# Performance work log

Measured on AMD Instinct MI355X. Metric: run time of the kernel, lower is better.

Reference implementation:

```python
import jax, jax.numpy as jnp
import numpy as np

N = 200000          # active input voxels
GRID = 96           # voxel grid extent
_OFFS = np.array([[dx, dy, dz] for dx in (-1, 0, 1) for dy in (-1, 0, 1) for dz in (-1, 0, 1)], dtype=np.int64)  # 27 kernel offsets


def _build_kmap(cin, cout, stride):
    """Build gather/scatter kernel maps for a 3x3x3 sparse conv.
    For each offset k and each output j, find input i with coord_in[i] == coord_out[j]*stride + off[k].
    Misses scatter to sentinel row n_out (dropped) and gather row 0 (value ignored)."""
    B = int(max(cin.max(), cout.max() * stride + 1)) + 3
    key_in = (cin[:, 0].astype(np.int64) * B + cin[:, 1]) * B + cin[:, 2]
    order = np.argsort(key_in).astype(np.int32)
    sk = key_in[order]
    n_out = cout.shape[0]
    g = np.zeros((27, n_out), np.int32)
    s = np.full((27, n_out), n_out, np.int32)
    ar = np.arange(n_out, dtype=np.int32)
    co = cout.astype(np.int64)
    for k in range(27):
        q = co * stride + _OFFS[k]
        valid = (q >= 0).all(axis=1)
        qk = (q[:, 0] * B + q[:, 1]) * B + q[:, 2]
        pos = np.clip(np.searchsorted(sk, qk), 0, sk.shape[0] - 1)
        found = valid & (sk[pos] == qk)
        g[k] = np.where(found, order[pos], 0)
        s[k] = np.where(found, ar, n_out)
    return jnp.asarray(g), jnp.asarray(s)


def setup_inputs() -> dict:
    rng = np.random.RandomState(0)
    raw = rng.randint(0, GRID, size=(3 * N, 3))
    coords = np.unique(raw, axis=0)[:N]          # [N,3] unique voxel coords
    c1 = coords
    c2 = np.unique(c1 // 2, axis=0)              # stride-2 output coords
    g1, s1 = _build_kmap(c1, c1, 1)              # submanifold conv1
    g2, s2 = _build_kmap(c1, c2, 2)              # strided conv2
    g3, s3 = _build_kmap(c2, c2, 1)              # submanifold conv3
    key = jax.random.key(0)
    k1, k2, k3, k4 = jax.random.split(key, 4)
    feats = jax.random.normal(k1, (N, 4), jnp.float32)
    W1 = jax.random.normal(k2, (27, 4, 32), jnp.float32) * (1.0 / np.sqrt(27 * 4))
    W2 = jax.random.normal(k3, (27, 32, 32), jnp.float32) * (1.0 / np.sqrt(27 * 32))
    W3 = jax.random.normal(k4, (27, 32, 2), jnp.float32) * (1.0 / np.sqrt(27 * 32))
    return {"feats": feats, "W1": W1, "W2": W2, "W3": W3,
            "g1": g1, "s1": s1, "g2": g2, "s2": s2, "g3": g3, "s3": s3}


def _sparse_conv(feats, W, gidx, sidx):
    n_out = sidx.shape[1]
    c_out = W.shape[-1]
    gathered = feats[gidx]                              # [27, M, Cin] irregular gather
    contrib = jnp.einsum('kmc,kcd->kmd', gathered, W)   # per-offset GEMM
    out = jnp.zeros((n_out + 1, c_out), feats.dtype)    # +1 sentinel row for misses
    out = out.at[sidx.reshape(-1)].add(contrib.reshape(-1, c_out))  # scatter-add
    return out[:n_out]


def reference(feats, W1, W2, W3, g1, s1, g2, s2, g3, s3):
    x = _sparse_conv(feats, W1, g1, s1)
    x = _sparse_conv(x, W2, g2, s2)
    x = _sparse_conv(x, W3, g3, s3)
    return x
```

## Files before the change

kernel.cpp:

```cpp
#include <hip/hip_runtime.h>

#define CDIV(a,b) (((a)+(b)-1)/(b))

typedef __attribute__((ext_vector_type(8))) short short8v;
typedef __attribute__((ext_vector_type(4))) short short4v;
typedef __attribute__((ext_vector_type(4))) float f32x4;

__device__ inline unsigned short f2bf(float x) {
    unsigned u = __builtin_bit_cast(unsigned, x);
    u += 0x7fffu + ((u >> 16) & 1u);
    return (unsigned short)(u >> 16);
}

__global__ __launch_bounds__(256) void prep_feats_k(
    const float* __restrict__ feats, unsigned short* __restrict__ featsh,
    unsigned short* __restrict__ x1h, int N)
{
    int i = blockIdx.x * 256 + threadIdx.x;
    if (i < N) {
        float4 f = *reinterpret_cast<const float4*>(feats + (size_t)i * 4);
        ushort4 h; h.x = f2bf(f.x); h.y = f2bf(f.y); h.z = f2bf(f.z); h.w = f2bf(f.w);
        *reinterpret_cast<ushort4*>(featsh + (size_t)i * 4) = h;
    } else if (i == N) {
        *reinterpret_cast<ushort4*>(featsh + (size_t)N * 4) = make_ushort4(0, 0, 0, 0);
        #pragma unroll
        for (int t = 0; t < 8; ++t)
            *reinterpret_cast<ushort4*>(x1h + (size_t)N * 32 + t * 4) = make_ushort4(0, 0, 0, 0);
    }
}

__global__ __launch_bounds__(256) void prep_w_k(
    const float* __restrict__ W1, const float* __restrict__ W2,
    unsigned short* __restrict__ w2h, unsigned short* __restrict__ w1f)
{
    int i = blockIdx.x * 256 + threadIdx.x;
    if (i < 27 * 1024) {
        int k = i >> 10, c = (i >> 5) & 31, d = i & 31;
        w2h[k * 1024 + d * 32 + c] = f2bf(W2[i]);
    } else if (i < 27 * 1024 + 4096) {
        int idx = i - 27 * 1024;
        int mf = idx >> 10, n = (idx >> 5) & 31, kc = idx & 31;
        int slot = mf * 8 + (kc >> 2), c = kc & 3;
        float v = (slot < 27) ? W1[slot * 128 + c * 32 + n] : 0.f;
        w1f[mf * 1024 + n * 32 + kc] = f2bf(v);
    }
}

__global__ __launch_bounds__(256, 6) void conv1_k(
    const unsigned short* __restrict__ featsh, const unsigned short* __restrict__ w1f,
    const int* __restrict__ g1, const int* __restrict__ s1,
    unsigned short* __restrict__ x1h, int N)
{
    int tid = threadIdx.x;
    int l = tid & 63, wv = tid >> 6;
    int lr = l & 15, kq = l >> 4;
    int rbase = blockIdx.x * 64 + wv * 16;
    int j = rbase + lr;
    int jc = j < N ? j : N - 1;

    int gm[4][2];
    #pragma unroll
    for (int mf = 0; mf < 4; ++mf)
        #pragma unroll
        for (int t = 0; t < 2; ++t) {
            int slot = mf * 8 + kq * 2 + t;
            int v = N;
            if (slot < 27 && j < N) {
                int s = s1[(size_t)slot * N + jc];
                int g = g1[(size_t)slot * N + jc];
                v = (s != N) ? g : N;
            }
            gm[mf][t] = v;
        }

    f32x4 acc0 = {0.f, 0.f, 0.f, 0.f}, acc1 = {0.f, 0.f, 0.f, 0.f};
    const char* fb = (const char*)featsh;
    const char* wb = (const char*)w1f;
    #pragma unroll
    for (int mf = 0; mf < 4; ++mf) {
        short4v lo = *(const short4v*)(fb + (size_t)gm[mf][0] * 8);
        short4v hi = *(const short4v*)(fb + (size_t)gm[mf][1] * 8);
        short8v a = __builtin_shufflevector(lo, hi, 0, 1, 2, 3, 4, 5, 6, 7);
        short8v b0 = *(const short8v*)(wb + mf * 2048 + lr * 64 + kq * 16);
        short8v b1 = *(const short8v*)(wb + mf * 2048 + 1024 + lr * 64 + kq * 16);
        acc0 = __builtin_amdgcn_mfma_f32_16x16x32_bf16(a, b0, acc0, 0, 0, 0);
        acc1 = __builtin_amdgcn_mfma_f32_16x16x32_bf16(a, b1, acc1, 0, 0, 0);
    }
    #pragma unroll
    for (int i = 0; i < 4; ++i) {
        int j2 = rbase + kq * 4 + i;
        if (j2 < N) {
            x1h[(size_t)j2 * 32 + lr]      = f2bf(acc0[i]);
            x1h[(size_t)j2 * 32 + lr + 16] = f2bf(acc1[i]);
        }
    }
}

__global__ __launch_bounds__(256, 6) void conv2_k(
    const unsigned short* __restrict__ x1h, const unsigned short* __restrict__ w2h,
    const int* __restrict__ g2, const int* __restrict__ s2,
    float* __restrict__ x2, int M, int N)
{
    int tid = threadIdx.x;
    int l = tid & 63, wv = tid >> 6;
    int lr = l & 15, kq = l >> 4;
    int rbase = blockIdx.x * 64 + wv * 16;
    int j = rbase + lr;
    int jc = j < M ? j : M - 1;

    int gm[27];
    #pragma unroll
    for (int k = 0; k < 27; ++k) {
        int s = s2[(size_t)k * M + jc];
        int g = g2[(size_t)k * M + jc];
        gm[k] = (s != M) ? g : N;
    }

    f32x4 acc0 = {0.f, 0.f, 0.f, 0.f}, acc1 = {0.f, 0.f, 0.f, 0.f};
    const char* xb = (const char*)x1h;
    const char* wb = (const char*)w2h;
    #pragma unroll
    for (int k = 0; k < 27; ++k) {
        short8v a  = *(const short8v*)(xb + (size_t)gm[k] * 64 + kq * 16);
        short8v b0 = *(const short8v*)(wb + k * 2048 + lr * 64 + kq * 16);
        short8v b1 = *(const short8v*)(wb + k * 2048 + 1024 + lr * 64 + kq * 16);
        acc0 = __builtin_amdgcn_mfma_f32_16x16x32_bf16(a, b0, acc0, 0, 0, 0);
        acc1 = __builtin_amdgcn_mfma_f32_16x16x32_bf16(a, b1, acc1, 0, 0, 0);
    }
    #pragma unroll
    for (int i = 0; i < 4; ++i) {
        int j2 = rbase + kq * 4 + i;
        if (j2 < M) {
            x2[(size_t)j2 * 32 + lr]      = acc0[i];
            x2[(size_t)j2 * 32 + lr + 16] = acc1[i];
        }
    }
}

__global__ __launch_bounds__(256, 6) void conv3_k(
    const float* __restrict__ x2, const float* __restrict__ W3,
    const int* __restrict__ g3, const int* __restrict__ s3,
    float* __restrict__ out, int M)
{
    __shared__ float w[27 * 64];
    int tid = threadIdx.x;
    for (int i = tid; i < 27 * 64; i += 256) w[i] = W3[i];
    __syncthreads();

    int q = tid & 3;
    int j = blockIdx.x * 64 + (tid >> 2);
    int jc = j < M ? j : M - 1;

    int gm[27];
    #pragma unroll
    for (int k = 0; k < 27; ++k) {
        int s = s3[(size_t)k * M + jc];
        int g = g3[(size_t)k * M + jc];
        gm[k] = (s != M) ? g : -1;
    }

    float a0 = 0.f, a1 = 0.f;
    #pragma unroll
    for (int k = 0; k < 27; ++k) {
        float m = gm[k] >= 0 ? 1.f : 0.f;
        int g = gm[k] >= 0 ? gm[k] : 0;
        const float* xr = x2 + (size_t)g * 32 + q * 8;
        float4 f0 = *(const float4*)(xr);
        float4 f1 = *(const float4*)(xr + 4);
        const float* wk = w + k * 64 + q * 16;
        float4 wA = *(const float4*)(wk);
        float4 wB = *(const float4*)(wk + 4);
        float4 wC = *(const float4*)(wk + 8);
        float4 wD = *(const float4*)(wk + 12);
        a0 += m * (f0.x * wA.x + f0.y * wA.z + f0.z * wB.x + f0.w * wB.z
                 + f1.x * wC.x + f1.y * wC.z + f1.z * wD.x + f1.w * wD.z);
        a1 += m * (f0.x * wA.y + f0.y * wA.w + f0.z * wB.y + f0.w * wB.w
                 + f1.x * wC.y + f1.y * wC.w + f1.z * wD.y + f1.w * wD.w);
    }
    a0 += __shfl_xor(a0, 1); a0 += __shfl_xor(a0, 2);
    a1 += __shfl_xor(a1, 1); a1 += __shfl_xor(a1, 2);
    if (q == 0 && j < M)
        *reinterpret_cast<float2*>(out + (size_t)j * 2) = make_float2(a0, a1);
}

extern "C" void kernel_launch(void* const* d_in, const int* in_sizes, int n_in,
                              void* d_out, int out_size, void* d_ws, size_t ws_size,
                              hipStream_t stream) {
    const float* feats = (const float*)d_in[0];
    const float* W1    = (const float*)d_in[1];
    const float* W2    = (const float*)d_in[2];
    const float* W3    = (const float*)d_in[3];
    const int*   g1    = (const int*)d_in[4];
    const int*   s1    = (const int*)d_in[5];
    const int*   g2    = (const int*)d_in[6];
    const int*   s2    = (const int*)d_in[7];
    const int*   g3    = (const int*)d_in[8];
    const int*   s3    = (const int*)d_in[9];

    int N = in_sizes[0] / 4;
    int M = in_sizes[6] / 27;

    char* wsb = (char*)d_ws;
    size_t off = 0;
    auto alloc = [&](size_t bytes) {
        char* p = wsb + off;
        off = (off + bytes + 255) & ~(size_t)255;
        return p;
    };
    unsigned short* x1h    = (unsigned short*)alloc((size_t)(N + 1) * 64);
    unsigned short* featsh = (unsigned short*)alloc((size_t)(N + 1) * 8);
    unsigned short* w2h    = (unsigned short*)alloc(27 * 1024 * 2);
    unsigned short* w1f    = (unsigned short*)alloc(4 * 1024 * 2);
    float*          x2     = (float*)alloc((size_t)M * 128);
    float* out = (float*)d_out;

    prep_feats_k<<<CDIV(N + 1, 256), 256, 0, stream>>>(feats, featsh, x1h, N);
    prep_w_k<<<CDIV(27 * 1024 + 4096, 256), 256, 0, stream>>>(W1, W2, w2h, w1f);
    conv1_k<<<CDIV(N, 64), 256, 0, stream>>>(featsh, w1f, g1, s1, x1h, N);
    conv2_k<<<CDIV(M, 64), 256, 0, stream>>>(x1h, w2h, g2, s2, x2, M, N);
    conv3_k<<<CDIV(M, 64), 256, 0, stream>>>(x2, W3, g3, s3, out, M);
}
```

Baseline: 171.0 us.

## Switch conv1 and conv2 to 32x32x16 MFMA tiles with 32 rows per wave

Replaces the paired 16x16x32 bf16 MFMAs in conv1 and conv2 with single 32x32x16 MFMAs, so each wave now handles 32 output rows and all 32 output channels in one accumulator. The W1 fragment layout is repacked to match, and blocks now cover 128 rows, halving the grid. The launch-bounds occupancy hint of 6 is dropped from the conv kernels. The aim is fewer MFMA issues and less redundant weight loading per output row, at the cost of a larger accumulator per wave and narrower scattered output stores.

```diff
diff --git a/kernel.cpp b/kernel.cpp
--- a/kernel.cpp
+++ b/kernel.cpp
@@ -2,9 +2,9 @@
 
 #define CDIV(a,b) (((a)+(b)-1)/(b))
 
-typedef __attribute__((ext_vector_type(8))) short short8v;
-typedef __attribute__((ext_vector_type(4))) short short4v;
-typedef __attribute__((ext_vector_type(4))) float f32x4;
+typedef __attribute__((ext_vector_type(8)))  short short8v;
+typedef __attribute__((ext_vector_type(4)))  short short4v;
+typedef __attribute__((ext_vector_type(16))) float f32x16;
 
 __device__ inline unsigned short f2bf(float x) {
     unsigned u = __builtin_bit_cast(unsigned, x);
@@ -39,73 +39,69 @@
         w2h[k * 1024 + d * 32 + c] = f2bf(W2[i]);
     } else if (i < 27 * 1024 + 4096) {
         int idx = i - 27 * 1024;
-        int mf = idx >> 10, n = (idx >> 5) & 31, kc = idx & 31;
-        int slot = mf * 8 + (kc >> 2), c = kc & 3;
+        int m = idx >> 9, n = (idx >> 4) & 31, kk = idx & 15;
+        int slot = 4 * m + (kk >> 2), c = kk & 3;
         float v = (slot < 27) ? W1[slot * 128 + c * 32 + n] : 0.f;
-        w1f[mf * 1024 + n * 32 + kc] = f2bf(v);
-    }
-}
-
-__global__ __launch_bounds__(256, 6) void conv1_k(
+        w1f[m * 512 + n * 16 + kk] = f2bf(v);
+    }
+}
+
+__global__ __launch_bounds__(256) void conv1_k(
     const unsigned short* __restrict__ featsh, const unsigned short* __restrict__ w1f,
     const int* __restrict__ g1, const int* __restrict__ s1,
     unsigned short* __restrict__ x1h, int N)
 {
     int tid = threadIdx.x;
     int l = tid & 63, wv = tid >> 6;
-    int lr = l & 15, kq = l >> 4;
-    int rbase = blockIdx.x * 64 + wv * 16;
-    int j = rbase + lr;
+    int r = l & 31, h = l >> 5;
+    int rbase = blockIdx.x * 128 + wv * 32;
+    int j = rbase + r;
     int jc = j < N ? j : N - 1;
 
-    int gm[4][2];
-    #pragma unroll
-    for (int mf = 0; mf < 4; ++mf)
+    int gm[8][2];
+    #pragma unroll
+    for (int m = 0; m < 8; ++m)
         #pragma unroll
         for (int t = 0; t < 2; ++t) {
-            int slot = mf * 8 + kq * 2 + t;
+            int slot = 4 * m + 2 * h + t;
             int v = N;
             if (slot < 27 && j < N) {
                 int s = s1[(size_t)slot * N + jc];
                 int g = g1[(size_t)slot * N + jc];
                 v = (s != N) ? g : N;
             }
-            gm[mf][t] = v;
+            gm[m][t] = v;
         }
 
-    f32x4 acc0 = {0.f, 0.f, 0.f, 0.f}, acc1 = {0.f, 0.f, 0.f, 0.f};
+    f32x16 acc = {};
     const char* fb = (const char*)featsh;
     const char* wb = (const char*)w1f;
     #pragma unroll
-    for (int mf = 0; mf < 4; ++mf) {
-        short4v lo = *(const short4v*)(fb + (size_t)gm[mf][0] * 8);
-        short4v hi = *(const short4v*)(fb + (size_t)gm[mf][1] * 8);
+    for (int m = 0; m < 8; ++m) {
+        short4v lo = *(const short4v*)(fb + (size_t)gm[m][0] * 8);
+        short4v hi = *(const short4v*)(fb + (size_t)gm[m][1] * 8);
         short8v a = __builtin_shufflevector(lo, hi, 0, 1, 2, 3, 4, 5, 6, 7);
-        short8v b0 = *(const short8v*)(wb + mf * 2048 + lr * 64 + kq * 16);
-        short8v b1 = *(const short8v*)(wb + mf * 2048 + 1024 + lr * 64 + kq * 16);
-        acc0 = __builtin_amdgcn_mfma_f32_16x16x32_bf16(a, b0, acc0, 0, 0, 0);
-        acc1 = __builtin_amdgcn_mfma_f32_16x16x32_bf16(a, b1, acc1, 0, 0, 0);
-    }
-    #pragma unroll
-    for (int i = 0; i < 4; ++i) {
-        int j2 = rbase + kq * 4 + i;
-        if (j2 < N) {
-            x1h[(size_t)j2 * 32 + lr]      = f2bf(acc0[i]);
-            x1h[(size_t)j2 * 32 + lr + 16] = f2bf(acc1[i]);
-        }
-    }
-}
-
-__global__ __launch_bounds__(256, 6) void conv2_k(
+        short8v b = *(const short8v*)(wb + (m * 512 + r * 16 + h * 8) * 2);
+        acc = __builtin_amdgcn_mfma_f32_32x32x16_bf16(a, b, acc, 0, 0, 0);
+    }
+    #pragma unroll
+    for (int reg = 0; reg < 16; ++reg) {
+        int row = (reg & 3) + 8 * (reg >> 2) + 4 * h;
+        int j2 = rbase + row;
+        if (j2 < N) x1h[(size_t)j2 * 32 + r] = f2bf(acc[reg]);
+    }
+}
+
+__global__ __launch_bounds__(256) void conv2_k(
     const unsigned short* __restrict__ x1h, const unsigned short* __restrict__ w2h,
     const int* __restrict__ g2, const int* __restrict__ s2,
     float* __restrict__ x2, int M, int N)
 {
     int tid = threadIdx.x;
     int l = tid & 63, wv = tid >> 6;
-    int lr = l & 15, kq = l >> 4;
-    int rbase = blockIdx.x * 64 + wv * 16;
-    int j = rbase + lr;
+    int r = l & 31, h = l >> 5;
+    int rbase = blockIdx.x * 128 + wv * 32;
+    int j = rbase + r;
     int jc = j < M ? j : M - 1;
 
     int gm[27];
@@ -113,31 +109,31 @@
     for (int k = 0; k < 27; ++k) {
         int s = s2[(size_t)k * M + jc];
         int g = g2[(size_t)k * M + jc];
-        gm[k] = (s != M) ? g : N;
-    }
-
-    f32x4 acc0 = {0.f, 0.f, 0.f, 0.f}, acc1 = {0.f, 0.f, 0.f, 0.f};
+        gm[k] = (j < M && s != M) ? g : N;
+    }
+
+    f32x16 acc = {};
     const char* xb = (const char*)x1h;
     const char* wb = (const char*)w2h;
     #pragma unroll
     for (int k = 0; k < 27; ++k) {
-        short8v a  = *(const short8v*)(xb + (size_t)gm[k] * 64 + kq * 16);
-        short8v b0 = *(const short8v*)(wb + k * 2048 + lr * 64 + kq * 16);
-        short8v b1 = *(const short8v*)(wb + k * 2048 + 1024 + lr * 64 + kq * 16);
-        acc0 = __builtin_amdgcn_mfma_f32_16x16x32_bf16(a, b0, acc0, 0, 0, 0);
-        acc1 = __builtin_amdgcn_mfma_f32_16x16x32_bf16(a, b1, acc1, 0, 0, 0);
-    }
-    #pragma unroll
-    for (int i = 0; i < 4; ++i) {
-        int j2 = rbase + kq * 4 + i;
-        if (j2 < M) {
-            x2[(size_t)j2 * 32 + lr]      = acc0[i];
-            x2[(size_t)j2 * 32 + lr + 16] = acc1[i];
-        }
-    }
-}
-
-__global__ __launch_bounds__(256, 6) void conv3_k(
+        const char* xr = xb + (size_t)gm[k] * 64;
+        short8v a0 = *(const short8v*)(xr + h * 16);
+        short8v a1 = *(const short8v*)(xr + 32 + h * 16);
+        short8v b0 = *(const short8v*)(wb + k * 2048 + r * 64 + h * 16);
+        short8v b1 = *(const short8v*)(wb + k * 2048 + r * 64 + 32 + h * 16);
+        acc = __builtin_amdgcn_mfma_f32_32x32x16_bf16(a0, b0, acc, 0, 0, 0);
+        acc = __builtin_amdgcn_mfma_f32_32x32x16_bf16(a1, b1, acc, 0, 0, 0);
+    }
+    #pragma unroll
+    for (int reg = 0; reg < 16; ++reg) {
+        int row = (reg & 3) + 8 * (reg >> 2) + 4 * h;
+        int j2 = rbase + row;
+        if (j2 < M) x2[(size_t)j2 * 32 + r] = acc[reg];
+    }
+}
+
+__global__ __launch_bounds__(256) void conv3_k(
     const float* __restrict__ x2, const float* __restrict__ W3,
     const int* __restrict__ g3, const int* __restrict__ s3,
     float* __restrict__ out, int M)
@@ -210,13 +206,13 @@
     unsigned short* x1h    = (unsigned short*)alloc((size_t)(N + 1) * 64);
     unsigned short* featsh = (unsigned short*)alloc((size_t)(N + 1) * 8);
     unsigned short* w2h    = (unsigned short*)alloc(27 * 1024 * 2);
-    unsigned short* w1f    = (unsigned short*)alloc(4 * 1024 * 2);
+    unsigned short* w1f    = (unsigned short*)alloc(8 * 512 * 2);
     float*          x2     = (float*)alloc((size_t)M * 128);
     float* out = (float*)d_out;
 
     prep_feats_k<<<CDIV(N + 1, 256), 256, 0, stream>>>(feats, featsh, x1h, N);
     prep_w_k<<<CDIV(27 * 1024 + 4096, 256), 256, 0, stream>>>(W1, W2, w2h, w1f);
-    conv1_k<<<CDIV(N, 64), 256, 0, stream>>>(featsh, w1f, g1, s1, x1h, N);
-    conv2_k<<<CDIV(M, 64), 256, 0, stream>>>(x1h, w2h, g2, s2, x2, M, N);
-    conv3_k<<<CDIV(M, 64), 256, 0, stream>>>(x2, W3, g3, s3, out, M);
-}
+    conv1_k<<<CDIV(N, 128), 256, 0, stream>>>(featsh, w1f, g1, s1, x1h, N);
+    conv2_k<<<CDIV(M, 128), 256, 0, stream>>>(x1h, w2h, g2, s2, x2, M, N);
+    conv3_k<<<CDIV(M, 64),  256, 0, stream>>>(x2, W3, g3, s3, out, M);
+}
```

Result: no change. 168.3 us (-1.6%).
